# Performance work log

Measured on AMD Instinct MI355X. Metric: run time of the kernel, lower is better.

Reference implementation:

```python
import jax, jax.numpy as jnp
import numpy as np

N, E = 10000, 320000
IN_CH, HID, OUT_CH, HEADS = 128, 64, 40, 8
NEG_SLOPE = 0.2


def gat_conv(x, src, dst, W, a_src, a_dst, bias, heads, C, concat, n_nodes):
    # x: [N, F_in]; W: [F_in, heads*C]; a_src/a_dst: [heads, C]
    h = (x @ W).reshape(n_nodes, heads, C)              # [N,H,C]
    alpha_src = jnp.sum(h * a_src, axis=-1)             # [N,H]
    alpha_dst = jnp.sum(h * a_dst, axis=-1)             # [N,H]
    score = jax.nn.leaky_relu(alpha_src[src] + alpha_dst[dst], NEG_SLOPE)  # [E,H]
    # segment softmax over edges sharing the same destination node
    smax = jax.ops.segment_max(score, dst, num_segments=n_nodes)
    smax = jnp.where(jnp.isfinite(smax), smax, 0.0)
    ex = jnp.exp(score - smax[dst])
    denom = jax.ops.segment_sum(ex, dst, num_segments=n_nodes)
    alpha = ex / (denom[dst] + 1e-16)                   # [E,H]
    msg = h[src] * alpha[:, :, None]                    # [E,H,C]
    out = jax.ops.segment_sum(msg, dst, num_segments=n_nodes)  # [N,H,C]
    out = out.reshape(n_nodes, heads * C) if concat else out.mean(axis=1)
    return out + bias


def setup_inputs() -> dict:
    key = jax.random.key(0)
    ks = jax.random.split(key, 16)
    g = 0.1
    return {
        "x": jax.random.normal(ks[0], (N, IN_CH), jnp.float32),
        "edge_index": jax.random.randint(ks[1], (2, E), 0, N, jnp.int64),
        "W1": jax.random.normal(ks[2], (IN_CH, HID), jnp.float32) * g,
        "b1": jnp.zeros((HID,), jnp.float32),
        "Wc1": jax.random.normal(ks[3], (HID, HEADS * HID), jnp.float32) * g,
        "att_src1": jax.random.normal(ks[4], (HEADS, HID), jnp.float32) * g,
        "att_dst1": jax.random.normal(ks[5], (HEADS, HID), jnp.float32) * g,
        "bc1": jnp.zeros((HEADS * HID,), jnp.float32),
        "Wc2": jax.random.normal(ks[6], (HEADS * HID, HID), jnp.float32) * g,
        "att_src2": jax.random.normal(ks[7], (1, HID), jnp.float32) * g,
        "att_dst2": jax.random.normal(ks[8], (1, HID), jnp.float32) * g,
        "bc2": jnp.zeros((HID,), jnp.float32),
        "W2": jax.random.normal(ks[9], (HID, OUT_CH), jnp.float32) * g,
        "b2": jnp.zeros((OUT_CH,), jnp.float32),
    }


def reference(x, edge_index, W1, b1, Wc1, att_src1, att_dst1, bc1,
              Wc2, att_src2, att_dst2, bc2, W2, b2):
    # add self-loops (PyG GATConv default add_self_loops=True)
    loop = jnp.arange(N, dtype=edge_index.dtype)
    src = jnp.concatenate([edge_index[0], loop])
    dst = jnp.concatenate([edge_index[1], loop])

    h = jax.nn.relu(x @ W1 + b1)                                   # lin0 + relu (dropout off in eval)
    h = jax.nn.elu(gat_conv(h, src, dst, Wc1, att_src1, att_dst1, bc1,
                            HEADS, HID, True, N))                  # conv1, concat heads
    h = gat_conv(h, src, dst, Wc2, att_src2, att_dst2, bc2,
                 1, HID, False, N)                                 # conv2, single head
    return h @ W2 + b2
```

## Files before the change

kernel.cpp:

```cpp
#include <hip/hip_runtime.h>
#include <cstdint>
#include <cstddef>

#define IN_CH 128
#define HID 64
#define HEADS 8
#define OUT_CH 40
#define NEG 0.2f
#define PAD 128

typedef __attribute__((ext_vector_type(8))) short bf16x8;
typedef __attribute__((ext_vector_type(4))) float f32x4;

#define MFMA(a, b, c) __builtin_amdgcn_mfma_f32_16x16x32_bf16(a, b, c, 0, 0, 0)

__device__ inline unsigned short f2bf(float f) {
    unsigned u = __float_as_uint(f);
    unsigned r = (u + 0x7FFFu + ((u >> 16) & 1u)) >> 16;
    return (unsigned short)r;
}
__device__ inline float bf2f(unsigned short b) {
    return __uint_as_float((unsigned)b << 16);
}
__device__ inline bf16x8 ldb8(const unsigned short* p) {
    return *reinterpret_cast<const bf16x8*>(p);
}


__global__ void k_init(const float* __restrict__ W1,
                       const float* __restrict__ Wc1, const float* __restrict__ Wc2,
                       const float* __restrict__ as1, const float* __restrict__ ad1,
                       int* __restrict__ cursor,
                       unsigned short* __restrict__ W1T,
                       unsigned short* __restrict__ Wc1T, unsigned short* __restrict__ Wc2T,
                       unsigned short* __restrict__ vaT, int N) {
    int i = blockIdx.x * 256 + threadIdx.x;
    if (i < N) { cursor[i] = 0; return; }
    i -= N;
    if (i < 64 * 128) {
        int j = i >> 7, k = i & 127;
        W1T[i] = f2bf(W1[k * 64 + j]);
        return;
    }
    i -= 64 * 128;
    if (i < 512 * 64) {
        int j = i >> 6, k = i & 63;
        Wc1T[i] = f2bf(Wc1[(size_t)k * 512 + j]);
        return;
    }
    i -= 512 * 64;
    if (i < 64 * 512) {
        int j = i >> 9, k = i & 511;
        Wc2T[i] = f2bf(Wc2[(size_t)k * 64 + j]);
        return;
    }
    i -= 64 * 512;
    if (i < 1024) {
        int t = i >> 6, k = i & 63;
        int h = t & 7;
        const float* a = (t < 8) ? as1 : ad1;
        float sum = 0.f;
        for (int c = 0; c < 64; ++c) sum += Wc1[(size_t)k * 512 + h * 64 + c] * a[h * 64 + c];
        vaT[t * 64 + k] = f2bf(sum);
    }
}


__global__ __launch_bounds__(256) void k_lin1m(const float* __restrict__ x,
                                               const unsigned short* __restrict__ W1T,
                                               const float* __restrict__ b1,
                                               const unsigned short* __restrict__ vaT,
                                               unsigned short* __restrict__ h0b,
                                               float* __restrict__ asrc, float* __restrict__ adst,
                                               const int* __restrict__ ei, int E, int T,
                                               int* __restrict__ cursor, int* __restrict__ csrc,
                                               int N, int NB) {
    __shared__ unsigned short h0s[16][72];
    if (blockIdx.x >= NB) {
        int e = (blockIdx.x - NB) * 256 + threadIdx.x;
        if (e < T) {
            int s, d;
            if (e < E) { s = ei[e]; d = ei[E + e]; } else { s = d = e - E; }
            int pos = atomicAdd(&cursor[d], 1);
            csrc[(size_t)d * PAD + pos] = s;
        }
        return;
    }
    int w = threadIdx.x >> 6, l = threadIdx.x & 63;
    int m0 = blockIdx.x * 16;
    int c = l & 15, g = l >> 4;
    int xr = m0 + c; if (xr >= N) xr = N - 1;
    bf16x8 af[4];
    const float* arow = x + (size_t)xr * 128 + 8 * g;
#pragma unroll
    for (int ks = 0; ks < 4; ++ks) {
        float4 f0 = *(const float4*)(arow + 32 * ks);
        float4 f1 = *(const float4*)(arow + 32 * ks + 4);
        bf16x8 t;
        t[0] = (short)f2bf(f0.x); t[1] = (short)f2bf(f0.y);
        t[2] = (short)f2bf(f0.z); t[3] = (short)f2bf(f0.w);
        t[4] = (short)f2bf(f1.x); t[5] = (short)f2bf(f1.y);
        t[6] = (short)f2bf(f1.z); t[7] = (short)f2bf(f1.w);
        af[ks] = t;
    }
    f32x4 acc = {};
    const unsigned short* brow = W1T + (size_t)(16 * w + c) * 128 + 8 * g;
#pragma unroll
    for (int ks = 0; ks < 4; ++ks) acc = MFMA(af[ks], ldb8(brow + 32 * ks), acc);
    int j = 16 * w + c;
    float bj = b1[j];
#pragma unroll
    for (int r = 0; r < 4; ++r) {
        float v = fmaxf(acc[r] + bj, 0.f);
        unsigned short us = f2bf(v);
        int row = m0 + 4 * g + r;
        if (row < N) h0b[(size_t)row * 64 + j] = us;
        h0s[4 * g + r][j] = us;
    }
    __syncthreads();
    if (w == 0) {
        bf16x8 a0 = ldb8(&h0s[c][8 * g]);
        bf16x8 a1 = ldb8(&h0s[c][32 + 8 * g]);
        bf16x8 b0 = ldb8(&vaT[c * 64 + 8 * g]);
        bf16x8 b1v = ldb8(&vaT[c * 64 + 32 + 8 * g]);
        f32x4 al = {};
        al = MFMA(a0, b0, al);
        al = MFMA(a1, b1v, al);
#pragma unroll
        for (int r = 0; r < 4; ++r) {
            int n = m0 + 4 * g + r;
            if (n < N) {
                if (c < 8) asrc[n * 8 + c] = al[r];
                else       adst[n * 8 + (c - 8)] = al[r];
            }
        }
    }
}


__global__ __launch_bounds__(128) void k_conv1agg(const unsigned short* __restrict__ h0b,
                                                  const float* __restrict__ asrc, const float* __restrict__ adst,
                                                  const int* __restrict__ degs, const int* __restrict__ csrc,
                                                  unsigned short* __restrict__ aggb, int N) {
    __shared__ int srcb[PAD];
    __shared__ float sb[PAD][8];
    __shared__ float mx[8], den[8], adl[8];
    __shared__ float accsh[512];
    int tid = threadIdx.x;
    int n = blockIdx.x;
    int deg = degs[n];
    if (tid < 8) adl[tid] = adst[n * 8 + tid];
    __syncthreads();
    if (tid < deg) {
        int s = csrc[(size_t)n * PAD + tid];
        srcb[tid] = s;
        const float4* ap = (const float4*)&asrc[(size_t)s * 8];
        float4 a0 = ap[0], a1 = ap[1];
        float v;
        v = a0.x + adl[0]; sb[tid][0] = (v >= 0.f) ? v : NEG * v;
        v = a0.y + adl[1]; sb[tid][1] = (v >= 0.f) ? v : NEG * v;
        v = a0.z + adl[2]; sb[tid][2] = (v >= 0.f) ? v : NEG * v;
        v = a0.w + adl[3]; sb[tid][3] = (v >= 0.f) ? v : NEG * v;
        v = a1.x + adl[4]; sb[tid][4] = (v >= 0.f) ? v : NEG * v;
        v = a1.y + adl[5]; sb[tid][5] = (v >= 0.f) ? v : NEG * v;
        v = a1.z + adl[6]; sb[tid][6] = (v >= 0.f) ? v : NEG * v;
        v = a1.w + adl[7]; sb[tid][7] = (v >= 0.f) ? v : NEG * v;
    }
    __syncthreads();
    if (tid < 64) {
        int hh = tid & 7, idx = tid >> 3;
        float m = -1e30f;
        for (int i = idx; i < deg; i += 8) m = fmaxf(m, sb[i][hh]);
        m = fmaxf(m, __shfl_xor(m, 8));
        m = fmaxf(m, __shfl_xor(m, 16));
        m = fmaxf(m, __shfl_xor(m, 32));
        if (tid < 8) mx[tid] = m;
    }
    __syncthreads();
    if (tid < 64) {
        int hh = tid & 7, idx = tid >> 3;
        float mh = mx[hh];
        float d = 0.f;
        for (int i = idx; i < deg; i += 8) {
            float e = __expf(sb[i][hh] - mh);
            sb[i][hh] = e;
            d += e;
        }
        d += __shfl_xor(d, 8);
        d += __shfl_xor(d, 16);
        d += __shfl_xor(d, 32);
        if (tid < 8) den[tid] = d + 1e-16f;
    }
    __syncthreads();
    int lane = tid & 63, wv = tid >> 6;
    int half = lane >> 5, cl = lane & 31;
    float accA[8] = {0.f, 0.f, 0.f, 0.f, 0.f, 0.f, 0.f, 0.f};
    float accB[8] = {0.f, 0.f, 0.f, 0.f, 0.f, 0.f, 0.f, 0.f};
    for (int i = 2 * wv; i < deg; i += 4) {
        int e = i + half;
        float vx = 0.f, vy = 0.f;
        float4 w0 = {0.f, 0.f, 0.f, 0.f}, w1 = {0.f, 0.f, 0.f, 0.f};
        if (e < deg) {
            unsigned u = *(const unsigned*)&h0b[(size_t)srcb[e] * 64 + 2 * cl];
            vx = bf2f((unsigned short)(u & 0xFFFFu));
            vy = bf2f((unsigned short)(u >> 16));
            w0 = *(const float4*)&sb[e][0];
            w1 = *(const float4*)&sb[e][4];
        }
        accA[0] += w0.x * vx; accB[0] += w0.x * vy;
        accA[1] += w0.y * vx; accB[1] += w0.y * vy;
        accA[2] += w0.z * vx; accB[2] += w0.z * vy;
        accA[3] += w0.w * vx; accB[3] += w0.w * vy;
        accA[4] += w1.x * vx; accB[4] += w1.x * vy;
        accA[5] += w1.y * vx; accB[5] += w1.y * vy;
        accA[6] += w1.z * vx; accB[6] += w1.z * vy;
        accA[7] += w1.w * vx; accB[7] += w1.w * vy;
    }
#pragma unroll
    for (int h = 0; h < 8; ++h) {
        accA[h] += __shfl_xor(accA[h], 32);
        accB[h] += __shfl_xor(accB[h], 32);
    }
    __syncthreads();
    if (wv == 1 && half == 0) {
#pragma unroll
        for (int h = 0; h < 8; ++h) {
            accsh[h * 64 + 2 * cl] = accA[h];
            accsh[h * 64 + 2 * cl + 1] = accB[h];
        }
    }
    __syncthreads();
    if (wv == 0 && half == 0) {
#pragma unroll
        for (int h = 0; h < 8; ++h) {
            float t0 = (accA[h] + accsh[h * 64 + 2 * cl]) / den[h];
            float t1 = (accB[h] + accsh[h * 64 + 2 * cl + 1]) / den[h];
            unsigned uo = (unsigned)f2bf(t0) | ((unsigned)f2bf(t1) << 16);
            *(unsigned*)&aggb[(size_t)n * 512 + h * 64 + 2 * cl] = uo;
        }
    }
}


__global__ __launch_bounds__(512) void k_p1l2(const unsigned short* __restrict__ aggb,
                                              const unsigned short* __restrict__ Wc1T,
                                              const float* __restrict__ bc1,
                                              const unsigned short* __restrict__ Wc2T,
                                              const float* __restrict__ as2, const float* __restrict__ ad2,
                                              unsigned short* __restrict__ hc2b,
                                              float* __restrict__ asrc, float* __restrict__ adst, int N) {
    __shared__ unsigned short h1s[16][520];
    __shared__ float part[7][4][64][4];
    int w = threadIdx.x >> 6, l = threadIdx.x & 63;
    int m0 = blockIdx.x * 16;
    int c = l & 15, g = l >> 4;
    {
        const unsigned short* arow = aggb + (size_t)(m0 + c) * 512 + w * 64 + 8 * g;
        bf16x8 af0 = ldb8(arow), af1 = ldb8(arow + 32);
        f32x4 acc[4] = {};
#pragma unroll
        for (int nt = 0; nt < 4; ++nt) {
            const unsigned short* brow = Wc1T + (size_t)(w * 64 + 16 * nt + c) * 64 + 8 * g;
            acc[nt] = MFMA(af0, ldb8(brow), acc[nt]);
            acc[nt] = MFMA(af1, ldb8(brow + 32), acc[nt]);
        }
#pragma unroll
        for (int nt = 0; nt < 4; ++nt) {
            int j = w * 64 + 16 * nt + c;
            float bj = bc1[j];
#pragma unroll
            for (int r = 0; r < 4; ++r) {
                float v = acc[nt][r] + bj;
                v = (v > 0.f) ? v : __expf(v) - 1.f;
                h1s[4 * g + r][j] = f2bf(v);
            }
        }
    }
    __syncthreads();
    f32x4 acc2[4] = {};
#pragma unroll
    for (int ks = 0; ks < 2; ++ks) {
        bf16x8 af = ldb8(&h1s[c][64 * w + 32 * ks + 8 * g]);
#pragma unroll
        for (int nt = 0; nt < 4; ++nt) {
            const unsigned short* brow = Wc2T + (size_t)(16 * nt + c) * 512 + 64 * w + 32 * ks + 8 * g;
            acc2[nt] = MFMA(af, ldb8(brow), acc2[nt]);
        }
    }
    if (w > 0) {
#pragma unroll
        for (int nt = 0; nt < 4; ++nt)
            *(f32x4*)&part[w - 1][nt][l][0] = acc2[nt];
    }
    __syncthreads();
    if (w != 0) return;
#pragma unroll
    for (int nt = 0; nt < 4; ++nt)
#pragma unroll
        for (int i = 0; i < 7; ++i) {
            f32x4 pp = *(const f32x4*)&part[i][nt][l][0];
            acc2[nt][0] += pp[0]; acc2[nt][1] += pp[1];
            acc2[nt][2] += pp[2]; acc2[nt][3] += pp[3];
        }
    float ps[4] = {0.f, 0.f, 0.f, 0.f}, pd[4] = {0.f, 0.f, 0.f, 0.f};
#pragma unroll
    for (int nt = 0; nt < 4; ++nt) {
        int j = 16 * nt + c;
        float aj = as2[j], dj = ad2[j];
#pragma unroll
        for (int r = 0; r < 4; ++r) {
            float v = acc2[nt][r];
            hc2b[(size_t)(m0 + 4 * g + r) * 64 + j] = f2bf(v);
            ps[r] += v * aj;
            pd[r] += v * dj;
        }
    }
#pragma unroll
    for (int r = 0; r < 4; ++r) {
        float s = ps[r], d = pd[r];
        s += __shfl_xor(s, 1); s += __shfl_xor(s, 2); s += __shfl_xor(s, 4); s += __shfl_xor(s, 8);
        d += __shfl_xor(d, 1); d += __shfl_xor(d, 2); d += __shfl_xor(d, 4); d += __shfl_xor(d, 8);
        if (c == 0) {
            int n = m0 + 4 * g + r;
            asrc[n] = s;
            adst[n] = d;
        }
    }
}


__global__ __launch_bounds__(256) void k_conv2f(const unsigned short* __restrict__ hc2b,
                                                const float* __restrict__ asrc, const float* __restrict__ adst,
                                                const int* __restrict__ degs, const int* __restrict__ csrc,
                                                const float* __restrict__ bc2,
                                                const float* __restrict__ W2, const float* __restrict__ b2,
                                                float* __restrict__ out, int N) {
    __shared__ float w2s[HID * OUT_CH];
    __shared__ float cosh_[4][HID];
    int tid = threadIdx.x;
    for (int i = tid; i < HID * OUT_CH; i += 256) w2s[i] = W2[i];
    int lane = tid & 63, nl = tid >> 6;
    int half = lane >> 5, cl = lane & 31;
    int n = blockIdx.x * 4 + nl;
    if (n < N) {
        int deg = degs[n];
        float ad = adst[n];
        float rm = -1e30f, rden = 0.f;
        float ax = 0.f, ay = 0.f;
        for (int base = 0; base < deg; base += 64) {
            int cnt = min(64, deg - base);
            int s = 0;
            float sc = -1e30f;
            if (lane < cnt) {
                s = csrc[(size_t)n * PAD + base + lane];
                float v = asrc[s] + ad;
                sc = (v >= 0.f) ? v : NEG * v;
            }
            float m = sc;
#pragma unroll
            for (int mm = 1; mm < 64; mm <<= 1) m = fmaxf(m, __shfl_xor(m, mm));
            float nmv = fmaxf(rm, m);
            float scale = __expf(rm - nmv);
            float p = (lane < cnt) ? __expf(sc - nmv) : 0.f;
            float d = p;
#pragma unroll
            for (int mm = 1; mm < 64; mm <<= 1) d += __shfl_xor(d, mm);
            rden = rden * scale + d;
            rm = nmv;
            ax *= scale; ay *= scale;
            for (int i = 0; i < cnt; i += 2) {
                int idx = i + half;
                float pi = __shfl(p, idx);
                int si = __shfl(s, idx);
                unsigned u = *(const unsigned*)&hc2b[(size_t)si * 64 + 2 * cl];
                ax += pi * bf2f((unsigned short)(u & 0xFFFFu));
                ay += pi * bf2f((unsigned short)(u >> 16));
            }
        }
        ax += __shfl_xor(ax, 32);
        ay += __shfl_xor(ay, 32);
        if (half == 0) {
            float inv = 1.f / (rden + 1e-16f);
            cosh_[nl][2 * cl] = ax * inv + bc2[2 * cl];
            cosh_[nl][2 * cl + 1] = ay * inv + bc2[2 * cl + 1];
        }
    }
    __syncthreads();
    if (tid >= 160) return;
    int nn = tid / 40, j = tid % 40;
    int no = blockIdx.x * 4 + nn;
    if (no >= N) return;
    float s = b2[j];
#pragma unroll 8
    for (int k = 0; k < HID; ++k) s += cosh_[nn][k] * w2s[k * OUT_CH + j];
    out[(size_t)no * OUT_CH + j] = s;
}


extern "C" void kernel_launch(void* const* d_in, const int* in_sizes, int n_in,
                              void* d_out, int out_size, void* d_ws, size_t ws_size,
                              hipStream_t stream) {
    const float* x   = (const float*)d_in[0];
    const int*   ei  = (const int*)d_in[1];
    const float* W1  = (const float*)d_in[2];
    const float* b1  = (const float*)d_in[3];
    const float* Wc1 = (const float*)d_in[4];
    const float* as1 = (const float*)d_in[5];
    const float* ad1 = (const float*)d_in[6];
    const float* bc1 = (const float*)d_in[7];
    const float* Wc2 = (const float*)d_in[8];
    const float* as2 = (const float*)d_in[9];
    const float* ad2 = (const float*)d_in[10];
    const float* bc2 = (const float*)d_in[11];
    const float* W2  = (const float*)d_in[12];
    const float* b2  = (const float*)d_in[13];

    const int N = in_sizes[0] / IN_CH;
    const int E = in_sizes[1] / 2;
    const int T = E + N;

    char* base = (char*)d_ws;
    size_t off = 0;
    auto carve = [&](size_t bytes) -> void* {
        off = (off + 255) & ~(size_t)255;
        void* r = base + off;
        off += bytes;
        return r;
    };
    int* cursor     = (int*)carve((size_t)N * 4);
    int* csrc       = (int*)carve((size_t)N * PAD * 4);
    unsigned short* W1T  = (unsigned short*)carve((size_t)64 * 128 * 2);
    unsigned short* Wc1T = (unsigned short*)carve((size_t)512 * 64 * 2);
    unsigned short* Wc2T = (unsigned short*)carve((size_t)64 * 512 * 2);
    unsigned short* vaT  = (unsigned short*)carve((size_t)16 * 64 * 2);
    unsigned short* h0b  = (unsigned short*)carve((size_t)N * 64 * 2);
    float* asrc1    = (float*)carve((size_t)N * 8 * 4);
    float* adst1    = (float*)carve((size_t)N * 8 * 4);
    unsigned short* aggb = (unsigned short*)carve((size_t)N * 512 * 2);
    unsigned short* hc2b = (unsigned short*)carve((size_t)N * 64 * 2);
    float* asrc2    = (float*)carve((size_t)N * 4);
    float* adst2    = (float*)carve((size_t)N * 4);

    int init_total = N + 64 * 128 + 512 * 64 + 64 * 512 + 1024;
    k_init<<<(init_total + 255) / 256, 256, 0, stream>>>(W1, Wc1, Wc2, as1, ad1, cursor,
                                                         W1T, Wc1T, Wc2T, vaT, N);

    int NB = (N + 15) / 16;
    int FB = (T + 255) / 256;
    k_lin1m<<<NB + FB, 256, 0, stream>>>(x, W1T, b1, vaT, h0b, asrc1, adst1,
                                         ei, E, T, cursor, csrc, N, NB);
    k_conv1agg<<<N, 128, 0, stream>>>(h0b, asrc1, adst1, cursor, csrc, aggb, N);
    k_p1l2<<<(N + 15) / 16, 512, 0, stream>>>(aggb, Wc1T, bc1, Wc2T, as2, ad2,
                                              hc2b, asrc2, adst2, N);
    k_conv2f<<<(N + 3) / 4, 256, 0, stream>>>(hc2b, asrc2, adst2, cursor, csrc, bc2, W2, b2,
                                              (float*)d_out, N);
}
```

Before: 96.56 us.

## Repartition k_p1l2 second GEMM across output columns to drop split-K reduction

After: 95.37 us. Within noise of the previous version (-1.2%).

```diff
diff --git a/kernel.cpp b/kernel.cpp
--- a/kernel.cpp
+++ b/kernel.cpp
@@ -242,7 +242,7 @@
 }
 
 
-__global__ __launch_bounds__(512) void k_p1l2(const unsigned short* __restrict__ aggb,
+__global__ __launch_bounds__(256) void k_p1l2(const unsigned short* __restrict__ aggb,
                                               const unsigned short* __restrict__ Wc1T,
                                               const float* __restrict__ bc1,
                                               const unsigned short* __restrict__ Wc2T,
@@ -250,23 +250,25 @@
                                               unsigned short* __restrict__ hc2b,
                                               float* __restrict__ asrc, float* __restrict__ adst, int N) {
     __shared__ unsigned short h1s[16][520];
-    __shared__ float part[7][4][64][4];
+    __shared__ float pps[4][16][2];
     int w = threadIdx.x >> 6, l = threadIdx.x & 63;
     int m0 = blockIdx.x * 16;
     int c = l & 15, g = l >> 4;
-    {
-        const unsigned short* arow = aggb + (size_t)(m0 + c) * 512 + w * 64 + 8 * g;
+#pragma unroll
+    for (int hl = 0; hl < 2; ++hl) {
+        int h = 2 * w + hl;
+        const unsigned short* arow = aggb + (size_t)(m0 + c) * 512 + h * 64 + 8 * g;
         bf16x8 af0 = ldb8(arow), af1 = ldb8(arow + 32);
         f32x4 acc[4] = {};
 #pragma unroll
         for (int nt = 0; nt < 4; ++nt) {
-            const unsigned short* brow = Wc1T + (size_t)(w * 64 + 16 * nt + c) * 64 + 8 * g;
+            const unsigned short* brow = Wc1T + (size_t)(h * 64 + 16 * nt + c) * 64 + 8 * g;
             acc[nt] = MFMA(af0, ldb8(brow), acc[nt]);
             acc[nt] = MFMA(af1, ldb8(brow + 32), acc[nt]);
         }
 #pragma unroll
         for (int nt = 0; nt < 4; ++nt) {
-            int j = w * 64 + 16 * nt + c;
+            int j = h * 64 + 16 * nt + c;
             float bj = bc1[j];
 #pragma unroll
             for (int r = 0; r < 4; ++r) {
@@ -277,43 +279,22 @@
         }
     }
     __syncthreads();
-    f32x4 acc2[4] = {};
-#pragma unroll
-    for (int ks = 0; ks < 2; ++ks) {
-        bf16x8 af = ldb8(&h1s[c][64 * w + 32 * ks + 8 * g]);
-#pragma unroll
-        for (int nt = 0; nt < 4; ++nt) {
-            const unsigned short* brow = Wc2T + (size_t)(16 * nt + c) * 512 + 64 * w + 32 * ks + 8 * g;
-            acc2[nt] = MFMA(af, ldb8(brow), acc2[nt]);
-        }
-    }
-    if (w > 0) {
-#pragma unroll
-        for (int nt = 0; nt < 4; ++nt)
-            *(f32x4*)&part[w - 1][nt][l][0] = acc2[nt];
-    }
-    __syncthreads();
-    if (w != 0) return;
-#pragma unroll
-    for (int nt = 0; nt < 4; ++nt)
-#pragma unroll
-        for (int i = 0; i < 7; ++i) {
-            f32x4 pp = *(const f32x4*)&part[i][nt][l][0];
-            acc2[nt][0] += pp[0]; acc2[nt][1] += pp[1];
-            acc2[nt][2] += pp[2]; acc2[nt][3] += pp[3];
-        }
-    float ps[4] = {0.f, 0.f, 0.f, 0.f}, pd[4] = {0.f, 0.f, 0.f, 0.f};
-#pragma unroll
-    for (int nt = 0; nt < 4; ++nt) {
-        int j = 16 * nt + c;
-        float aj = as2[j], dj = ad2[j];
-#pragma unroll
-        for (int r = 0; r < 4; ++r) {
-            float v = acc2[nt][r];
-            hc2b[(size_t)(m0 + 4 * g + r) * 64 + j] = f2bf(v);
-            ps[r] += v * aj;
-            pd[r] += v * dj;
-        }
+    f32x4 acc2 = {};
+    const unsigned short* brow2 = Wc2T + (size_t)(16 * w + c) * 512 + 8 * g;
+#pragma unroll 4
+    for (int ks = 0; ks < 16; ++ks) {
+        bf16x8 af = ldb8(&h1s[c][32 * ks + 8 * g]);
+        acc2 = MFMA(af, ldb8(brow2 + 32 * ks), acc2);
+    }
+    int j = 16 * w + c;
+    float aj = as2[j], dj = ad2[j];
+    float ps[4], pd[4];
+#pragma unroll
+    for (int r = 0; r < 4; ++r) {
+        float v = acc2[r];
+        hc2b[(size_t)(m0 + 4 * g + r) * 64 + j] = f2bf(v);
+        ps[r] = v * aj;
+        pd[r] = v * dj;
     }
 #pragma unroll
     for (int r = 0; r < 4; ++r) {
@@ -321,9 +302,19 @@
         s += __shfl_xor(s, 1); s += __shfl_xor(s, 2); s += __shfl_xor(s, 4); s += __shfl_xor(s, 8);
         d += __shfl_xor(d, 1); d += __shfl_xor(d, 2); d += __shfl_xor(d, 4); d += __shfl_xor(d, 8);
         if (c == 0) {
-            int n = m0 + 4 * g + r;
-            asrc[n] = s;
-            adst[n] = d;
+            pps[w][4 * g + r][0] = s;
+            pps[w][4 * g + r][1] = d;
+        }
+    }
+    __syncthreads();
+    int tid = threadIdx.x;
+    if (tid < 32) {
+        int row = tid >> 1, sel = tid & 1;
+        float sum = pps[0][row][sel] + pps[1][row][sel] + pps[2][row][sel] + pps[3][row][sel];
+        int n = m0 + row;
+        if (n < N) {
+            if (sel == 0) asrc[n] = sum;
+            else          adst[n] = sum;
         }
     }
 }
@@ -450,7 +441,7 @@
     k_lin1m<<<NB + FB, 256, 0, stream>>>(x, W1T, b1, vaT, h0b, asrc1, adst1,
                                          ei, E, T, cursor, csrc, N, NB);
     k_conv1agg<<<N, 128, 0, stream>>>(h0b, asrc1, adst1, cursor, csrc, aggb, N);
-    k_p1l2<<<(N + 15) / 16, 512, 0, stream>>>(aggb, Wc1T, bc1, Wc2T, as2, ad2,
+    k_p1l2<<<(N + 15) / 16, 256, 0, stream>>>(aggb, Wc1T, bc1, Wc2T, as2, ad2,
                                               hc2b, asrc2, adst2, N);
     k_conv2f<<<(N + 3) / 4, 256, 0, stream>>>(hc2b, asrc2, adst2, cursor, csrc, bc2, W2, b2,
                                               (float*)d_out, N);
```
